# Optimization experiments

Measured on AMD Instinct MI355X. Metric: run time of the kernel, lower is better.

The kernel has to match this reference:

```python
import jax, jax.numpy as jnp
import numpy as np

NV, NE, D, NNZ = 100000, 50000, 128, 1600000
EPS = 1e-5

def _seg_mean(vals, idx, n):
    # vals: [nnz, d] gathered rows; mean-aggregate into n segments
    s = jax.ops.segment_sum(vals, idx, num_segments=n)
    c = jax.ops.segment_sum(jnp.ones((idx.shape[0], 1), vals.dtype), idx, num_segments=n)
    return s / jnp.maximum(c, 1.0)

def _linear(x, W, b):
    return x @ W.T + b

def _layer_norm(x, g, b):
    m = jnp.mean(x, axis=-1, keepdims=True)
    v = jnp.mean((x - m) ** 2, axis=-1, keepdims=True)
    return (x - m) * jax.lax.rsqrt(v + EPS) * g + b

def setup_inputs() -> dict:
    key = jax.random.key(0)
    ks = jax.random.split(key, 12)
    inp = {
        "X": jax.random.normal(ks[0], (NV, D), jnp.float32),
        "Y": jax.random.normal(ks[1], (NE, D), jnp.float32),
        "v_idx": jax.random.randint(ks[2], (NNZ,), 0, NV, jnp.int32),
        "e_idx": jax.random.randint(ks[3], (NNZ,), 0, NE, jnp.int32),
        "W_tv": jax.random.normal(ks[4], (D, D), jnp.float32) * 0.05,
        "b_tv": jnp.zeros((D,), jnp.float32),
        "W_te": jax.random.normal(ks[5], (D, D), jnp.float32) * 0.05,
        "b_te": jnp.zeros((D,), jnp.float32),
        "W_em": jax.random.normal(ks[6], (D, 2 * D), jnp.float32) * 0.05,
        "b_em": jnp.zeros((D,), jnp.float32),
        "W_vm": jax.random.normal(ks[7], (D, 2 * D), jnp.float32) * 0.05,
        "b_vm": jnp.zeros((D,), jnp.float32),
        "g_v": jnp.ones((D,), jnp.float32),
        "be_v": jnp.zeros((D,), jnp.float32),
        "g_e": jnp.ones((D,), jnp.float32),
        "be_e": jnp.zeros((D,), jnp.float32),
    }
    return inp

def reference(X, Y, v_idx, e_idx, W_tv, b_tv, W_te, b_te, W_em, b_em, W_vm, b_vm, g_v, be_v, g_e, be_e):
    X0, Y0 = X, Y
    Xp = _linear(X0, W_tv, b_tv)                       # [NV, D] theta_vertex
    # v2e aggregation (mean): gather vertex rows per incidence, reduce to edges
    msg_e = _seg_mean(Xp[v_idx], e_idx, NE)            # [NE, D]
    Ym = _linear(jnp.concatenate([Y0, msg_e], axis=-1), W_em, b_em)  # edge_merge
    Ym = _linear(Ym, W_te, b_te)                       # theta_edge
    # e2v aggregation (mean)
    msg_v = _seg_mean(Ym[e_idx], v_idx, NV)            # [NV, D]
    Xm = _linear(jnp.concatenate([X0, msg_v], axis=-1), W_vm, b_vm)  # vertex_merge
    Xo = jax.nn.relu(_layer_norm(Xm, g_v, be_v))       # dropout is identity at eval / p=0
    Yo = jax.nn.relu(_layer_norm(Ym, g_e, be_e))
    return (Xo, Yo)
```

## Files before the change

kernel.cpp:

```cpp
#include <hip/hip_runtime.h>
#include <stdint.h>

#define NVERT 100000
#define NEDGE 50000
#define DIM 128
#define NNZ_N 1600000
#define N4 (NNZ_N / 4)
#define CAP_E 96
#define NB_QTR 1563
#define LDS_STRIDE 136

typedef __attribute__((ext_vector_type(8))) short bf16x8;
typedef __attribute__((ext_vector_type(4))) float f32x4;

__device__ __forceinline__ unsigned short f32_to_bf16(float f) {
  union { float f; unsigned u; } v; v.f = f;
  unsigned r = v.u + 0x7fffu + ((v.u >> 16) & 1u);
  return (unsigned short)(r >> 16);
}
__device__ __forceinline__ float bf16_lo(unsigned u) {
  union { unsigned u; float f; } v; v.u = u << 16; return v.f;
}
__device__ __forceinline__ float bf16_hi(unsigned u) {
  union { unsigned u; float f; } v; v.u = u & 0xffff0000u; return v.f;
}
__device__ __forceinline__ float ldf(const void* p, long i, int bf) {
  if (bf) {
    union { unsigned u; float f; } v;
    v.u = (unsigned)((const unsigned short*)p)[i] << 16;
    return v.f;
  }
  return ((const float*)p)[i];
}
__device__ __forceinline__ bf16x8 frag_ext(const void* A, long idx, int bf) {
  if (bf) return *(const bf16x8*)((const unsigned short*)A + idx);
  const float* f = (const float*)A + idx;
  float4 f0 = *(const float4*)f, f1 = *(const float4*)(f + 4);
  bf16x8 r;
  r[0] = (short)f32_to_bf16(f0.x); r[1] = (short)f32_to_bf16(f0.y);
  r[2] = (short)f32_to_bf16(f0.z); r[3] = (short)f32_to_bf16(f0.w);
  r[4] = (short)f32_to_bf16(f1.x); r[5] = (short)f32_to_bf16(f1.y);
  r[6] = (short)f32_to_bf16(f1.z); r[7] = (short)f32_to_bf16(f1.w);
  return r;
}

__device__ __forceinline__ int block_flag(const unsigned short* x) {
  __shared__ int cnt;
  if (threadIdx.x == 0) cnt = 0;
  __syncthreads();
  int c = 0;
#pragma unroll
  for (int k = 0; k < 4; ++k) {
    unsigned short h = x[(threadIdx.x * 4 + k) * 2];
    int ex = (h >> 7) & 0xFF;
    c += (ex >= 100 && ex <= 140) ? 1 : 0;
  }
  atomicAdd(&cnt, c);
  __syncthreads();
  return cnt > 512;
}

__global__ __launch_bounds__(256) void prep_all(
    const unsigned short* __restrict__ Xu,
    const void* __restrict__ btv, const void* __restrict__ bvm,
    const void* __restrict__ Wtv, const void* __restrict__ Wvm,
    const void* __restrict__ Wte, const void* __restrict__ Wem,
    const void* __restrict__ bte, const void* __restrict__ bem,
    float* __restrict__ btvf, float* __restrict__ bvmf, float* __restrict__ bcf,
    unsigned short* __restrict__ Wtvb, unsigned short* __restrict__ Wvmb,
    unsigned short* __restrict__ Wcb, int* __restrict__ flag,
    int* __restrict__ cnt_e, int* __restrict__ cnt_v) {
  int b = blockIdx.x, t = threadIdx.x;
  if (b >= 321) {
    int i = (b - 321) * 256 + t;
    if (i < NEDGE) cnt_e[i] = 0;
    else if (i < NEDGE + NVERT) cnt_v[i - NEDGE] = 0;
    return;
  }
  int bf = block_flag(Xu);
  if (b == 0) {
    if (t == 0) flag[0] = bf;
    if (t < 128) btvf[t] = ldf(btv, t, bf);
    else bvmf[t - 128] = ldf(bvm, t - 128, bf);
  } else if (b < 65) {
    int i = (b - 1) * 256 + t;
    Wtvb[i] = f32_to_bf16(ldf(Wtv, i, bf));
  } else if (b < 193) {
    int i = (b - 65) * 256 + t;
    Wvmb[i] = f32_to_bf16(ldf(Wvm, i, bf));
  } else {
    int n = b - 193, k = t;
    float acc = 0.f;
    for (int j = 0; j < 128; ++j)
      acc += ldf(Wte, n * 128 + j, bf) * ldf(Wem, j * 256 + k, bf);
    Wcb[n * 256 + k] = f32_to_bf16(acc);
    if (k == 0) {
      float bb = ldf(bte, n, bf);
      for (int j = 0; j < 128; ++j) bb += ldf(Wte, n * 128 + j, bf) * ldf(bem, j, bf);
      bcf[n] = bb;
    }
  }
}

__device__ __forceinline__ void ecount_body(
    const int4* __restrict__ vi, const int4* __restrict__ ei,
    int* __restrict__ cnt_e, int* __restrict__ adj_e, int bid) {
  int i = bid * 256 + threadIdx.x;
  if (i >= N4) return;
  int4 e = ei[i], v = vi[i];
  int t;
  t = atomicAdd(&cnt_e[e.x], 1); if (t < CAP_E) adj_e[e.x * CAP_E + t] = v.x;
  t = atomicAdd(&cnt_e[e.y], 1); if (t < CAP_E) adj_e[e.y * CAP_E + t] = v.y;
  t = atomicAdd(&cnt_e[e.z], 1); if (t < CAP_E) adj_e[e.z * CAP_E + t] = v.z;
  t = atomicAdd(&cnt_e[e.w], 1); if (t < CAP_E) adj_e[e.w * CAP_E + t] = v.w;
}

__device__ __forceinline__ void vcount_body(
    const int4* __restrict__ vi, int* __restrict__ cnt_v,
    int4* __restrict__ tV, int bid) {
  int i = bid * 256 + threadIdx.x;
  if (i >= N4) return;
  int4 v = vi[i];
  int4 tv;
  tv.x = atomicAdd(&cnt_v[v.x], 1);
  tv.y = atomicAdd(&cnt_v[v.y], 1);
  tv.z = atomicAdd(&cnt_v[v.z], 1);
  tv.w = atomicAdd(&cnt_v[v.w], 1);
  tV[i] = tv;
}

__global__ __launch_bounds__(256) void k_wadjv(
    const int4* __restrict__ vi, const int4* __restrict__ ei,
    const int4* __restrict__ tV, const int* __restrict__ off_v,
    const int* __restrict__ bsum, int* __restrict__ adj_v) {
  int i = blockIdx.x * 256 + threadIdx.x;
  if (i >= N4) return;
  int4 e = ei[i], v = vi[i], tv = tV[i];
  adj_v[off_v[v.x] + bsum[v.x >> 10] + tv.x] = e.x;
  adj_v[off_v[v.y] + bsum[v.y >> 10] + tv.y] = e.y;
  adj_v[off_v[v.z] + bsum[v.z >> 10] + tv.z] = e.z;
  adj_v[off_v[v.w] + bsum[v.w >> 10] + tv.w] = e.w;
}

__global__ __launch_bounds__(1024) void scan_block(const int* __restrict__ in,
                                                   int* __restrict__ out,
                                                   int* __restrict__ bsum, int n) {
  __shared__ int sd[1024];
  const int tid = threadIdx.x;
  const int i = blockIdx.x * 1024 + tid;
  int x = (i < n) ? in[i] : 0;
  sd[tid] = x;
  __syncthreads();
  int v = x;
  for (int s = 1; s < 1024; s <<= 1) {
    int t = (tid >= s) ? sd[tid - s] : 0;
    __syncthreads();
    v += t;
    sd[tid] = v;
    __syncthreads();
  }
  if (i < n) out[i] = v - x;
  if (tid == 1023) bsum[blockIdx.x] = v;
}

__global__ __launch_bounds__(1024) void scan_sums(int* __restrict__ bsum, int nb) {
  __shared__ int sd[1024];
  const int tid = threadIdx.x;
  int x = (tid < nb) ? bsum[tid] : 0;
  sd[tid] = x;
  __syncthreads();
  int v = x;
  for (int s = 1; s < 1024; s <<= 1) {
    int t = (tid >= s) ? sd[tid - s] : 0;
    __syncthreads();
    v += t;
    sd[tid] = v;
    __syncthreads();
  }
  if (tid < nb) bsum[tid] = v - x;
}

template<bool CAPMODE>
__device__ __forceinline__ void seg_to_lds(
    const int* __restrict__ off_or_cnt, const int* __restrict__ bsum, int total,
    const int* __restrict__ adj, const unsigned short* __restrict__ tbl,
    unsigned short* __restrict__ lds, int nseg, int nrows, int blk) {
  const int g = threadIdx.x >> 4;
  const int l = threadIdx.x & 15;
#pragma unroll
  for (int t = 0; t < 4; ++t) {
    const int seg_local = t * 16 + g;
    const int seg = blk * 64 + seg_local;
    if (seg < nseg) {
      int s, e, cnt;
      if (CAPMODE) {
        cnt = off_or_cnt[seg];
        s = seg * CAP_E;
        e = s + (cnt < CAP_E ? cnt : CAP_E);
      } else {
        s = off_or_cnt[seg] + bsum[seg >> 10];
        e = (seg + 1 < nseg) ? off_or_cnt[seg + 1] + bsum[(seg + 1) >> 10] : total;
        cnt = e - s;
      }
      float a0 = 0, a1 = 0, a2 = 0, a3 = 0, a4 = 0, a5 = 0, a6 = 0, a7 = 0;
#define ACC(u)                                         \
  a0 += bf16_lo(u.x); a1 += bf16_hi(u.x);              \
  a2 += bf16_lo(u.y); a3 += bf16_hi(u.y);              \
  a4 += bf16_lo(u.z); a5 += bf16_hi(u.z);              \
  a6 += bf16_lo(u.w); a7 += bf16_hi(u.w);
      int i = s;
      for (; i + 4 <= e; i += 4) {
        int r0 = adj[i], r1 = adj[i + 1], r2 = adj[i + 2], r3 = adj[i + 3];
        if ((unsigned)r0 >= (unsigned)nrows) r0 = 0;
        if ((unsigned)r1 >= (unsigned)nrows) r1 = 0;
        if ((unsigned)r2 >= (unsigned)nrows) r2 = 0;
        if ((unsigned)r3 >= (unsigned)nrows) r3 = 0;
        uint4 u0 = *(const uint4*)(tbl + (long)r0 * DIM + l * 8);
        uint4 u1 = *(const uint4*)(tbl + (long)r1 * DIM + l * 8);
        uint4 u2 = *(const uint4*)(tbl + (long)r2 * DIM + l * 8);
        uint4 u3 = *(const uint4*)(tbl + (long)r3 * DIM + l * 8);
        ACC(u0) ACC(u1) ACC(u2) ACC(u3)
      }
      for (; i < e; ++i) {
        int r = adj[i];
        if ((unsigned)r >= (unsigned)nrows) r = 0;
        uint4 u = *(const uint4*)(tbl + (long)r * DIM + l * 8);
        ACC(u)
      }
#undef ACC
      float inv = (cnt > 0) ? 1.f / (float)cnt : 0.f;
      bf16x8 r;
      r[0] = (short)f32_to_bf16(a0 * inv); r[1] = (short)f32_to_bf16(a1 * inv);
      r[2] = (short)f32_to_bf16(a2 * inv); r[3] = (short)f32_to_bf16(a3 * inv);
      r[4] = (short)f32_to_bf16(a4 * inv); r[5] = (short)f32_to_bf16(a5 * inv);
      r[6] = (short)f32_to_bf16(a6 * inv); r[7] = (short)f32_to_bf16(a7 * inv);
      *(bf16x8*)&lds[seg_local * LDS_STRIDE + l * 8] = r;
    }
  }
  __syncthreads();
}

template<int KSTEPS, bool STORE_BF16>
__device__ __forceinline__ void gemm_body(
    int bid, const void* __restrict__ A0,
    const unsigned short* __restrict__ Bw, const float* __restrict__ biasf,
    unsigned short* __restrict__ outb, int M, int bf) {
  constexpr int K = KSTEPS * 32;
  const int wave = threadIdx.x >> 6;
  const int lane = threadIdx.x & 63;
  const int m0 = bid * 64 + wave * 16;
  if (m0 >= M) return;
  const int c = lane & 15;
  const int q = lane >> 4;
  const long arow = m0 + c;

  f32x4 acc[8];
#pragma unroll
  for (int t = 0; t < 8; ++t) acc[t] = (f32x4){0.f, 0.f, 0.f, 0.f};
#pragma unroll
  for (int ks = 0; ks < KSTEPS; ++ks) {
    const int kk = ks * 32 + q * 8;
    bf16x8 a = frag_ext(A0, arow * (long)K + kk, bf);
#pragma unroll
    for (int t = 0; t < 8; ++t) {
      bf16x8 b = *(const bf16x8*)(Bw + (long)(t * 16 + c) * K + kk);
      acc[t] = __builtin_amdgcn_mfma_f32_16x16x32_bf16(a, b, acc[t], 0, 0, 0);
    }
  }
#pragma unroll
  for (int t = 0; t < 8; ++t) {
    float bv = biasf[t * 16 + c];
#pragma unroll
    for (int i = 0; i < 4; ++i) acc[t][i] += bv;
  }
  if (STORE_BF16) {
#pragma unroll
    for (int t = 0; t < 8; ++t) {
      int col = t * 16 + c;
#pragma unroll
      for (int i = 0; i < 4; ++i)
        outb[(long)(m0 + q * 4 + i) * DIM + col] = f32_to_bf16(acc[t][i]);
    }
  }
}

template<bool STORE_BF16>
__device__ __forceinline__ void gemm_lds_body(
    int bid, const void* __restrict__ A0, const unsigned short* __restrict__ lds,
    const unsigned short* __restrict__ Bw, const float* __restrict__ biasf,
    unsigned short* __restrict__ outb, float* __restrict__ outf,
    const void* __restrict__ gw_, const void* __restrict__ bw_,
    int M, int bf) {
  constexpr int K = 256;
  const int wave = threadIdx.x >> 6;
  const int lane = threadIdx.x & 63;
  const int m0 = bid * 64 + wave * 16;
  if (m0 >= M) return;
  const int c = lane & 15;
  const int q = lane >> 4;
  const long arow = m0 + c;
  const int rloc = wave * 16 + c;

  f32x4 acc[8];
#pragma unroll
  for (int t = 0; t < 8; ++t) acc[t] = (f32x4){0.f, 0.f, 0.f, 0.f};
#pragma unroll
  for (int ks = 0; ks < 8; ++ks) {
    const int kk = ks * 32 + q * 8;
    bf16x8 a;
    if (ks >= 4) a = *(const bf16x8*)&lds[rloc * LDS_STRIDE + (kk - 128)];
    else         a = frag_ext(A0, arow * 128 + kk, bf);
#pragma unroll
    for (int t = 0; t < 8; ++t) {
      bf16x8 b = *(const bf16x8*)(Bw + (long)(t * 16 + c) * K + kk);
      acc[t] = __builtin_amdgcn_mfma_f32_16x16x32_bf16(a, b, acc[t], 0, 0, 0);
    }
  }
#pragma unroll
  for (int t = 0; t < 8; ++t) {
    float bv = biasf[t * 16 + c];
#pragma unroll
    for (int i = 0; i < 4; ++i) acc[t][i] += bv;
  }
  if (STORE_BF16) {
#pragma unroll
    for (int t = 0; t < 8; ++t) {
      int col = t * 16 + c;
#pragma unroll
      for (int i = 0; i < 4; ++i)
        outb[(long)(m0 + q * 4 + i) * DIM + col] = f32_to_bf16(acc[t][i]);
    }
  }
  float sum[4] = {0, 0, 0, 0}, sq[4] = {0, 0, 0, 0};
#pragma unroll
  for (int t = 0; t < 8; ++t)
#pragma unroll
    for (int i = 0; i < 4; ++i) { float v = acc[t][i]; sum[i] += v; sq[i] += v * v; }
#pragma unroll
  for (int m = 1; m <= 8; m <<= 1) {
#pragma unroll
    for (int i = 0; i < 4; ++i) {
      sum[i] += __shfl_xor(sum[i], m, 64);
      sq[i]  += __shfl_xor(sq[i], m, 64);
    }
  }
  float mean[4], rstd[4];
#pragma unroll
  for (int i = 0; i < 4; ++i) {
    mean[i] = sum[i] * (1.0f / 128.0f);
    float var = sq[i] * (1.0f / 128.0f) - mean[i] * mean[i];
    rstd[i] = rsqrtf(var + 1e-5f);
  }
#pragma unroll
  for (int t = 0; t < 8; ++t) {
    int col = t * 16 + c;
    float gv = ldf(gw_, col, bf), bv = ldf(bw_, col, bf);
#pragma unroll
    for (int i = 0; i < 4; ++i) {
      float v = (acc[t][i] - mean[i]) * rstd[i] * gv + bv;
      v = v > 0.f ? v : 0.f;
      outf[(long)(m0 + q * 4 + i) * DIM + col] = v;
    }
  }
}

__global__ __launch_bounds__(256) void k_ecount_gemm1(
    const int4* __restrict__ vi, const int4* __restrict__ ei,
    int* __restrict__ cnt_e, int* __restrict__ adj_e,
    const void* __restrict__ X, const unsigned short* __restrict__ Wtvb,
    const float* __restrict__ btvf, unsigned short* __restrict__ Xp_b,
    const int* __restrict__ flagp) {
  if (blockIdx.x & 1)
    gemm_body<4, true>(blockIdx.x >> 1, X, Wtvb, btvf, Xp_b, NVERT, *flagp);
  else
    ecount_body(vi, ei, cnt_e, adj_e, blockIdx.x >> 1);
}

__global__ __launch_bounds__(256) void k_vcount_seg1gemm2(
    const int4* __restrict__ vi, int* __restrict__ cnt_v, int4* __restrict__ tV,
    const int* __restrict__ cnt_e, const int* __restrict__ adj_e,
    const unsigned short* __restrict__ Xp_b,
    const void* __restrict__ Y, const unsigned short* __restrict__ Wcb,
    const float* __restrict__ bcf, unsigned short* __restrict__ Ym_b,
    float* __restrict__ Yo, const void* __restrict__ g_e,
    const void* __restrict__ be_e, const int* __restrict__ flagp) {
  __shared__ unsigned short lds[64 * LDS_STRIDE];
  int r = blockIdx.x % 3, q = blockIdx.x / 3;
  if (r < 2) {
    vcount_body(vi, cnt_v, tV, q * 2 + r);
    return;
  }
  seg_to_lds<true>(cnt_e, nullptr, 0, adj_e, Xp_b, lds, NEDGE, NVERT, q);
  gemm_lds_body<true>(q, Y, lds, Wcb, bcf, Ym_b, Yo, g_e, be_e, NEDGE, *flagp);
}

__global__ __launch_bounds__(256) void k_seg2gemm3(
    const int* __restrict__ off_v, const int* __restrict__ bsum,
    const int* __restrict__ adj_v, const unsigned short* __restrict__ Ym_b,
    const void* __restrict__ X, const unsigned short* __restrict__ Wvmb,
    const float* __restrict__ bvmf, float* __restrict__ Xo,
    const void* __restrict__ g_v, const void* __restrict__ be_v,
    const int* __restrict__ flagp) {
  __shared__ unsigned short lds[64 * LDS_STRIDE];
  seg_to_lds<false>(off_v, bsum, NNZ_N, adj_v, Ym_b, lds, NVERT, NEDGE, blockIdx.x);
  gemm_lds_body<false>(blockIdx.x, X, lds, Wvmb, bvmf, nullptr, Xo, g_v, be_v,
                       NVERT, *flagp);
}

extern "C" void kernel_launch(void* const* d_in, const int* in_sizes, int n_in,
                              void* d_out, int out_size, void* d_ws, size_t ws_size,
                              hipStream_t stream) {
  const void* X    = d_in[0];
  const void* Y    = d_in[1];
  const int*  v_idx = (const int*)d_in[2];
  const int*  e_idx = (const int*)d_in[3];
  const void* W_tv = d_in[4];
  const void* b_tv = d_in[5];
  const void* W_te = d_in[6];
  const void* b_te = d_in[7];
  const void* W_em = d_in[8];
  const void* b_em = d_in[9];
  const void* W_vm = d_in[10];
  const void* b_vm = d_in[11];
  const void* g_v  = d_in[12];
  const void* be_v = d_in[13];
  const void* g_e  = d_in[14];
  const void* be_e = d_in[15];

  unsigned short* Xp_b = (unsigned short*)d_out;
  int*   adj_e = (int*)((char*)d_out + 25600000);
  int4*  tV4   = (int4*)((char*)d_out + 44800000);
  float* Yo    = (float*)d_out + (long)NVERT * DIM;
  float* Xo    = (float*)d_out;

  char* p = (char*)d_ws;
  auto alloc = [&](size_t n) { char* r = p; p += (n + 255) & ~(size_t)255; return r; };
  int*   flag  = (int*)alloc(4);
  float* btv_f = (float*)alloc(DIM * 4);
  float* bvm_f = (float*)alloc(DIM * 4);
  float* bc_f  = (float*)alloc(DIM * 4);
  unsigned short* Wtv_b = (unsigned short*)alloc(DIM * DIM * 2);
  unsigned short* Wvm_b = (unsigned short*)alloc(2 * DIM * DIM * 2);
  unsigned short* Wc_b  = (unsigned short*)alloc(2 * DIM * DIM * 2);
  unsigned short* Ym_b  = (unsigned short*)alloc((long)NEDGE * DIM * 2);
  int* off_v  = (int*)alloc((NVERT + 1) * 4);
  int* cnt_e  = (int*)alloc(NEDGE * 4);
  int* cnt_v  = (int*)alloc(NVERT * 4);
  int* bsum_v = (int*)alloc(((NVERT + 1023) / 1024) * 4);
  int* adj_v  = (int*)alloc((long)NNZ_N * 4);

  prep_all<<<321 + (NEDGE + NVERT + 255) / 256, 256, 0, stream>>>(
      (const unsigned short*)X, b_tv, b_vm, W_tv, W_vm, W_te, W_em, b_te, b_em,
      btv_f, bvm_f, bc_f, Wtv_b, Wvm_b, Wc_b, flag, cnt_e, cnt_v);

  k_ecount_gemm1<<<2 * NB_QTR, 256, 0, stream>>>(
      (const int4*)v_idx, (const int4*)e_idx, cnt_e, adj_e,
      X, Wtv_b, btv_f, Xp_b, flag);

  k_vcount_seg1gemm2<<<3 * ((NEDGE + 63) / 64), 256, 0, stream>>>(
      (const int4*)v_idx, cnt_v, tV4, cnt_e, adj_e, Xp_b,
      Y, Wc_b, bc_f, Ym_b, Yo, g_e, be_e, flag);

  {
    int nbv = (NVERT + 1023) / 1024;
    scan_block<<<nbv, 1024, 0, stream>>>(cnt_v, off_v, bsum_v, NVERT);
    scan_sums<<<1, 1024, 0, stream>>>(bsum_v, nbv);
  }

  k_wadjv<<<NB_QTR, 256, 0, stream>>>(
      (const int4*)v_idx, (const int4*)e_idx, tV4, off_v, bsum_v, adj_v);

  k_seg2gemm3<<<(NVERT + 63) / 64, 256, 0, stream>>>(
      off_v, bsum_v, adj_v, Ym_b, X, Wvm_b, bvm_f, Xo, g_v, be_v, flag);
}
```

Baseline: 580.7 us.

## Split segment-mean from GEMMs via global message buffers and rebalance kernel fusion

Decouples the gather/mean aggregation from the merge GEMMs. Aggregated messages now go to global bf16 buffers placed in unused regions of the output, instead of LDS tiles inside a fused seg+GEMM block. The kernels are regrouped so independent work runs side by side: weight prep overlaps the first GEMM and edge counting, the edge GEMM overlaps writing the vertex adjacency, and half of the vertex GEMM overlaps the second half of vertex aggregation. The gather loop is also unrolled to 8 rows per iteration to keep more loads in flight. The cost is an extra global round-trip for the messages, more launches, and careful aliasing of output memory.

```diff
diff --git a/kernel.cpp b/kernel.cpp
--- a/kernel.cpp
+++ b/kernel.cpp
@@ -8,7 +8,8 @@
 #define N4 (NNZ_N / 4)
 #define CAP_E 96
 #define NB_QTR 1563
-#define LDS_STRIDE 136
+#define NB_G23 782
+#define MSG_STRIDE 256
 
 typedef __attribute__((ext_vector_type(8))) short bf16x8;
 typedef __attribute__((ext_vector_type(4))) float f32x4;
@@ -60,19 +61,16 @@
   return cnt > 512;
 }
 
-__global__ __launch_bounds__(256) void prep_all(
+__global__ __launch_bounds__(256) void prep0(
     const unsigned short* __restrict__ Xu,
     const void* __restrict__ btv, const void* __restrict__ bvm,
-    const void* __restrict__ Wtv, const void* __restrict__ Wvm,
-    const void* __restrict__ Wte, const void* __restrict__ Wem,
-    const void* __restrict__ bte, const void* __restrict__ bem,
-    float* __restrict__ btvf, float* __restrict__ bvmf, float* __restrict__ bcf,
-    unsigned short* __restrict__ Wtvb, unsigned short* __restrict__ Wvmb,
-    unsigned short* __restrict__ Wcb, int* __restrict__ flag,
+    const void* __restrict__ Wtv,
+    float* __restrict__ btvf, float* __restrict__ bvmf,
+    unsigned short* __restrict__ Wtvb, int* __restrict__ flag,
     int* __restrict__ cnt_e, int* __restrict__ cnt_v) {
   int b = blockIdx.x, t = threadIdx.x;
-  if (b >= 321) {
-    int i = (b - 321) * 256 + t;
+  if (b >= 65) {
+    int i = (b - 65) * 256 + t;
     if (i < NEDGE) cnt_e[i] = 0;
     else if (i < NEDGE + NVERT) cnt_v[i - NEDGE] = 0;
     return;
@@ -82,14 +80,23 @@
     if (t == 0) flag[0] = bf;
     if (t < 128) btvf[t] = ldf(btv, t, bf);
     else bvmf[t - 128] = ldf(bvm, t - 128, bf);
-  } else if (b < 65) {
+  } else {
     int i = (b - 1) * 256 + t;
     Wtvb[i] = f32_to_bf16(ldf(Wtv, i, bf));
-  } else if (b < 193) {
-    int i = (b - 65) * 256 + t;
+  }
+}
+
+__device__ __forceinline__ void prep_wc_body(
+    int b, const void* __restrict__ Wvm, const void* __restrict__ Wte,
+    const void* __restrict__ Wem, const void* __restrict__ bte,
+    const void* __restrict__ bem, unsigned short* __restrict__ Wvmb,
+    unsigned short* __restrict__ Wcb, float* __restrict__ bcf, int bf) {
+  int t = threadIdx.x;
+  if (b < 128) {
+    int i = b * 256 + t;
     Wvmb[i] = f32_to_bf16(ldf(Wvm, i, bf));
   } else {
-    int n = b - 193, k = t;
+    int n = b - 128, k = t;
     float acc = 0.f;
     for (int j = 0; j < 128; ++j)
       acc += ldf(Wte, n * 128 + j, bf) * ldf(Wem, j * 256 + k, bf);
@@ -129,11 +136,11 @@
   tV[i] = tv;
 }
 
-__global__ __launch_bounds__(256) void k_wadjv(
+__device__ __forceinline__ void wadjv_body(
     const int4* __restrict__ vi, const int4* __restrict__ ei,
     const int4* __restrict__ tV, const int* __restrict__ off_v,
-    const int* __restrict__ bsum, int* __restrict__ adj_v) {
-  int i = blockIdx.x * 256 + threadIdx.x;
+    const int* __restrict__ bsum, int* __restrict__ adj_v, int bid) {
+  int i = bid * 256 + threadIdx.x;
   if (i >= N4) return;
   int4 e = ei[i], v = vi[i], tv = tV[i];
   adj_v[off_v[v.x] + bsum[v.x >> 10] + tv.x] = e.x;
@@ -181,71 +188,65 @@
 }
 
 template<bool CAPMODE>
-__device__ __forceinline__ void seg_to_lds(
-    const int* __restrict__ off_or_cnt, const int* __restrict__ bsum, int total,
-    const int* __restrict__ adj, const unsigned short* __restrict__ tbl,
-    unsigned short* __restrict__ lds, int nseg, int nrows, int blk) {
-  const int g = threadIdx.x >> 4;
+__device__ __forceinline__ void seg_body(
+    const int* __restrict__ off_or_cnt, const int* __restrict__ adj,
+    const unsigned short* __restrict__ tbl, unsigned short* __restrict__ out,
+    int nseg, int nrows, const int* __restrict__ bsum, int total, int bid) {
+  const int seg = (bid * 256 + threadIdx.x) >> 4;
   const int l = threadIdx.x & 15;
-#pragma unroll
-  for (int t = 0; t < 4; ++t) {
-    const int seg_local = t * 16 + g;
-    const int seg = blk * 64 + seg_local;
-    if (seg < nseg) {
-      int s, e, cnt;
-      if (CAPMODE) {
-        cnt = off_or_cnt[seg];
-        s = seg * CAP_E;
-        e = s + (cnt < CAP_E ? cnt : CAP_E);
-      } else {
-        s = off_or_cnt[seg] + bsum[seg >> 10];
-        e = (seg + 1 < nseg) ? off_or_cnt[seg + 1] + bsum[(seg + 1) >> 10] : total;
-        cnt = e - s;
-      }
-      float a0 = 0, a1 = 0, a2 = 0, a3 = 0, a4 = 0, a5 = 0, a6 = 0, a7 = 0;
+  if (seg >= nseg) return;
+  int s, e, cnt;
+  if (CAPMODE) {
+    cnt = off_or_cnt[seg];
+    s = seg * CAP_E;
+    e = s + (cnt < CAP_E ? cnt : CAP_E);
+  } else {
+    s = off_or_cnt[seg] + bsum[seg >> 10];
+    e = (seg + 1 < nseg) ? off_or_cnt[seg + 1] + bsum[(seg + 1) >> 10] : total;
+    cnt = e - s;
+  }
+  float a0 = 0, a1 = 0, a2 = 0, a3 = 0, a4 = 0, a5 = 0, a6 = 0, a7 = 0;
+#define ROW(r, u)                                      \
+  if ((unsigned)r >= (unsigned)nrows) r = 0;           \
+  uint4 u = *(const uint4*)(tbl + (long)r * DIM + l * 8);
 #define ACC(u)                                         \
   a0 += bf16_lo(u.x); a1 += bf16_hi(u.x);              \
   a2 += bf16_lo(u.y); a3 += bf16_hi(u.y);              \
   a4 += bf16_lo(u.z); a5 += bf16_hi(u.z);              \
   a6 += bf16_lo(u.w); a7 += bf16_hi(u.w);
-      int i = s;
-      for (; i + 4 <= e; i += 4) {
-        int r0 = adj[i], r1 = adj[i + 1], r2 = adj[i + 2], r3 = adj[i + 3];
-        if ((unsigned)r0 >= (unsigned)nrows) r0 = 0;
-        if ((unsigned)r1 >= (unsigned)nrows) r1 = 0;
-        if ((unsigned)r2 >= (unsigned)nrows) r2 = 0;
-        if ((unsigned)r3 >= (unsigned)nrows) r3 = 0;
-        uint4 u0 = *(const uint4*)(tbl + (long)r0 * DIM + l * 8);
-        uint4 u1 = *(const uint4*)(tbl + (long)r1 * DIM + l * 8);
-        uint4 u2 = *(const uint4*)(tbl + (long)r2 * DIM + l * 8);
-        uint4 u3 = *(const uint4*)(tbl + (long)r3 * DIM + l * 8);
-        ACC(u0) ACC(u1) ACC(u2) ACC(u3)
-      }
-      for (; i < e; ++i) {
-        int r = adj[i];
-        if ((unsigned)r >= (unsigned)nrows) r = 0;
-        uint4 u = *(const uint4*)(tbl + (long)r * DIM + l * 8);
-        ACC(u)
-      }
+  int i = s;
+  for (; i + 8 <= e; i += 8) {
+    int r0 = adj[i],     r1 = adj[i + 1], r2 = adj[i + 2], r3 = adj[i + 3];
+    int r4 = adj[i + 4], r5 = adj[i + 5], r6 = adj[i + 6], r7 = adj[i + 7];
+    ROW(r0, u0) ROW(r1, u1) ROW(r2, u2) ROW(r3, u3)
+    ROW(r4, u4) ROW(r5, u5) ROW(r6, u6) ROW(r7, u7)
+    ACC(u0) ACC(u1) ACC(u2) ACC(u3) ACC(u4) ACC(u5) ACC(u6) ACC(u7)
+  }
+  for (; i + 4 <= e; i += 4) {
+    int r0 = adj[i], r1 = adj[i + 1], r2 = adj[i + 2], r3 = adj[i + 3];
+    ROW(r0, u0) ROW(r1, u1) ROW(r2, u2) ROW(r3, u3)
+    ACC(u0) ACC(u1) ACC(u2) ACC(u3)
+  }
+  for (; i < e; ++i) {
+    int r = adj[i];
+    ROW(r, u)
+    ACC(u)
+  }
 #undef ACC
-      float inv = (cnt > 0) ? 1.f / (float)cnt : 0.f;
-      bf16x8 r;
-      r[0] = (short)f32_to_bf16(a0 * inv); r[1] = (short)f32_to_bf16(a1 * inv);
-      r[2] = (short)f32_to_bf16(a2 * inv); r[3] = (short)f32_to_bf16(a3 * inv);
-      r[4] = (short)f32_to_bf16(a4 * inv); r[5] = (short)f32_to_bf16(a5 * inv);
-      r[6] = (short)f32_to_bf16(a6 * inv); r[7] = (short)f32_to_bf16(a7 * inv);
-      *(bf16x8*)&lds[seg_local * LDS_STRIDE + l * 8] = r;
-    }
-  }
-  __syncthreads();
-}
-
-template<int KSTEPS, bool STORE_BF16>
-__device__ __forceinline__ void gemm_body(
+#undef ROW
+  float inv = (cnt > 0) ? 1.f / (float)cnt : 0.f;
+  bf16x8 r;
+  r[0] = (short)f32_to_bf16(a0 * inv); r[1] = (short)f32_to_bf16(a1 * inv);
+  r[2] = (short)f32_to_bf16(a2 * inv); r[3] = (short)f32_to_bf16(a3 * inv);
+  r[4] = (short)f32_to_bf16(a4 * inv); r[5] = (short)f32_to_bf16(a5 * inv);
+  r[6] = (short)f32_to_bf16(a6 * inv); r[7] = (short)f32_to_bf16(a7 * inv);
+  *(bf16x8*)(out + (long)seg * MSG_STRIDE + l * 8) = r;
+}
+
+__device__ __forceinline__ void gemm1_body(
     int bid, const void* __restrict__ A0,
     const unsigned short* __restrict__ Bw, const float* __restrict__ biasf,
     unsigned short* __restrict__ outb, int M, int bf) {
-  constexpr int K = KSTEPS * 32;
   const int wave = threadIdx.x >> 6;
   const int lane = threadIdx.x & 63;
   const int m0 = bid * 64 + wave * 16;
@@ -253,53 +254,43 @@
   const int c = lane & 15;
   const int q = lane >> 4;
   const long arow = m0 + c;
-
   f32x4 acc[8];
 #pragma unroll
   for (int t = 0; t < 8; ++t) acc[t] = (f32x4){0.f, 0.f, 0.f, 0.f};
 #pragma unroll
-  for (int ks = 0; ks < KSTEPS; ++ks) {
+  for (int ks = 0; ks < 4; ++ks) {
     const int kk = ks * 32 + q * 8;
-    bf16x8 a = frag_ext(A0, arow * (long)K + kk, bf);
+    bf16x8 a = frag_ext(A0, arow * 128 + kk, bf);
 #pragma unroll
     for (int t = 0; t < 8; ++t) {
-      bf16x8 b = *(const bf16x8*)(Bw + (long)(t * 16 + c) * K + kk);
+      bf16x8 b = *(const bf16x8*)(Bw + (long)(t * 16 + c) * 128 + kk);
       acc[t] = __builtin_amdgcn_mfma_f32_16x16x32_bf16(a, b, acc[t], 0, 0, 0);
     }
   }
 #pragma unroll
   for (int t = 0; t < 8; ++t) {
     float bv = biasf[t * 16 + c];
-#pragma unroll
-    for (int i = 0; i < 4; ++i) acc[t][i] += bv;
-  }
-  if (STORE_BF16) {
-#pragma unroll
-    for (int t = 0; t < 8; ++t) {
-      int col = t * 16 + c;
-#pragma unroll
-      for (int i = 0; i < 4; ++i)
-        outb[(long)(m0 + q * 4 + i) * DIM + col] = f32_to_bf16(acc[t][i]);
-    }
+    int col = t * 16 + c;
+#pragma unroll
+    for (int i = 0; i < 4; ++i)
+      outb[(long)(m0 + q * 4 + i) * DIM + col] = f32_to_bf16(acc[t][i] + bv);
   }
 }
 
 template<bool STORE_BF16>
-__device__ __forceinline__ void gemm_lds_body(
-    int bid, const void* __restrict__ A0, const unsigned short* __restrict__ lds,
+__device__ __forceinline__ void gemm23_body(
+    int bid, int rowbase, int M,
+    const void* __restrict__ A0, const unsigned short* __restrict__ A1b,
     const unsigned short* __restrict__ Bw, const float* __restrict__ biasf,
     unsigned short* __restrict__ outb, float* __restrict__ outf,
-    const void* __restrict__ gw_, const void* __restrict__ bw_,
-    int M, int bf) {
-  constexpr int K = 256;
+    const void* __restrict__ gw_, const void* __restrict__ bw_, int bf) {
   const int wave = threadIdx.x >> 6;
   const int lane = threadIdx.x & 63;
-  const int m0 = bid * 64 + wave * 16;
+  const int m0 = rowbase + bid * 64 + wave * 16;
   if (m0 >= M) return;
   const int c = lane & 15;
   const int q = lane >> 4;
   const long arow = m0 + c;
-  const int rloc = wave * 16 + c;
 
   f32x4 acc[8];
 #pragma unroll
@@ -308,11 +299,11 @@
   for (int ks = 0; ks < 8; ++ks) {
     const int kk = ks * 32 + q * 8;
     bf16x8 a;
-    if (ks >= 4) a = *(const bf16x8*)&lds[rloc * LDS_STRIDE + (kk - 128)];
+    if (ks >= 4) a = *(const bf16x8*)(A1b + arow * MSG_STRIDE + (kk - 128));
     else         a = frag_ext(A0, arow * 128 + kk, bf);
 #pragma unroll
     for (int t = 0; t < 8; ++t) {
-      bf16x8 b = *(const bf16x8*)(Bw + (long)(t * 16 + c) * K + kk);
+      bf16x8 b = *(const bf16x8*)(Bw + (long)(t * 16 + c) * 256 + kk);
       acc[t] = __builtin_amdgcn_mfma_f32_16x16x32_bf16(a, b, acc[t], 0, 0, 0);
     }
   }
@@ -364,47 +355,89 @@
   }
 }
 
-__global__ __launch_bounds__(256) void k_ecount_gemm1(
+__global__ __launch_bounds__(256) void k1_prep_ecount_gemm1(
     const int4* __restrict__ vi, const int4* __restrict__ ei,
     int* __restrict__ cnt_e, int* __restrict__ adj_e,
     const void* __restrict__ X, const unsigned short* __restrict__ Wtvb,
     const float* __restrict__ btvf, unsigned short* __restrict__ Xp_b,
+    const void* __restrict__ Wvm, const void* __restrict__ Wte,
+    const void* __restrict__ Wem, const void* __restrict__ bte,
+    const void* __restrict__ bem, unsigned short* __restrict__ Wvmb,
+    unsigned short* __restrict__ Wcb, float* __restrict__ bcf,
     const int* __restrict__ flagp) {
-  if (blockIdx.x & 1)
-    gemm_body<4, true>(blockIdx.x >> 1, X, Wtvb, btvf, Xp_b, NVERT, *flagp);
+  int b = blockIdx.x;
+  if (b < 256) {
+    prep_wc_body(b, Wvm, Wte, Wem, bte, bem, Wvmb, Wcb, bcf, *flagp);
+    return;
+  }
+  int b2 = b - 256;
+  if (b2 & 1)
+    gemm1_body(b2 >> 1, X, Wtvb, btvf, Xp_b, NVERT, *flagp);
   else
-    ecount_body(vi, ei, cnt_e, adj_e, blockIdx.x >> 1);
-}
-
-__global__ __launch_bounds__(256) void k_vcount_seg1gemm2(
+    ecount_body(vi, ei, cnt_e, adj_e, b2 >> 1);
+}
+
+__global__ __launch_bounds__(256) void k2_vcount_seg1(
     const int4* __restrict__ vi, int* __restrict__ cnt_v, int4* __restrict__ tV,
     const int* __restrict__ cnt_e, const int* __restrict__ adj_e,
-    const unsigned short* __restrict__ Xp_b,
-    const void* __restrict__ Y, const unsigned short* __restrict__ Wcb,
-    const float* __restrict__ bcf, unsigned short* __restrict__ Ym_b,
-    float* __restrict__ Yo, const void* __restrict__ g_e,
-    const void* __restrict__ be_e, const int* __restrict__ flagp) {
-  __shared__ unsigned short lds[64 * LDS_STRIDE];
+    const unsigned short* __restrict__ Xp_b, unsigned short* __restrict__ msg_e) {
   int r = blockIdx.x % 3, q = blockIdx.x / 3;
-  if (r < 2) {
-    vcount_body(vi, cnt_v, tV, q * 2 + r);
-    return;
-  }
-  seg_to_lds<true>(cnt_e, nullptr, 0, adj_e, Xp_b, lds, NEDGE, NVERT, q);
-  gemm_lds_body<true>(q, Y, lds, Wcb, bcf, Ym_b, Yo, g_e, be_e, NEDGE, *flagp);
-}
-
-__global__ __launch_bounds__(256) void k_seg2gemm3(
+  if (r == 0)
+    vcount_body(vi, cnt_v, tV, q);
+  else
+    seg_body<true>(cnt_e, adj_e, Xp_b, msg_e, NEDGE, NVERT, nullptr, 0,
+                   q * 2 + (r - 1));
+}
+
+__global__ __launch_bounds__(256) void k3_wadjv_gemm2(
+    const int4* __restrict__ vi, const int4* __restrict__ ei,
+    const int4* __restrict__ tV, const int* __restrict__ off_v,
+    const int* __restrict__ bsum, int* __restrict__ adj_v,
+    const void* __restrict__ Y, const unsigned short* __restrict__ msg_e,
+    const unsigned short* __restrict__ Wcb, const float* __restrict__ bcf,
+    unsigned short* __restrict__ Ym_b, float* __restrict__ Yo,
+    const void* __restrict__ g_e, const void* __restrict__ be_e,
+    const int* __restrict__ flagp) {
+  int r = blockIdx.x % 3, q = blockIdx.x / 3;
+  if (r == 2)
+    gemm23_body<true>(q, 0, NEDGE, Y, msg_e, Wcb, bcf, Ym_b, Yo, g_e, be_e,
+                      *flagp);
+  else
+    wadjv_body(vi, ei, tV, off_v, bsum, adj_v, q * 2 + r);
+}
+
+__global__ __launch_bounds__(256) void k4a_seg2(
     const int* __restrict__ off_v, const int* __restrict__ bsum,
     const int* __restrict__ adj_v, const unsigned short* __restrict__ Ym_b,
+    unsigned short* __restrict__ msg_v) {
+  seg_body<false>(off_v, adj_v, Ym_b, msg_v, NVERT, NEDGE, bsum, NNZ_N,
+                  blockIdx.x);
+}
+
+__global__ __launch_bounds__(256) void k4b_seg2_gemm3(
+    const int* __restrict__ off_v, const int* __restrict__ bsum,
+    const int* __restrict__ adj_v, const unsigned short* __restrict__ Ym_b,
+    unsigned short* __restrict__ msg_v,
     const void* __restrict__ X, const unsigned short* __restrict__ Wvmb,
     const float* __restrict__ bvmf, float* __restrict__ Xo,
     const void* __restrict__ g_v, const void* __restrict__ be_v,
     const int* __restrict__ flagp) {
-  __shared__ unsigned short lds[64 * LDS_STRIDE];
-  seg_to_lds<false>(off_v, bsum, NNZ_N, adj_v, Ym_b, lds, NVERT, NEDGE, blockIdx.x);
-  gemm_lds_body<false>(blockIdx.x, X, lds, Wvmb, bvmf, nullptr, Xo, g_v, be_v,
-                       NVERT, *flagp);
+  int r = blockIdx.x % 5, q = blockIdx.x / 5;
+  if (r == 4)
+    gemm23_body<false>(q, 0, NVERT / 2, X, msg_v, Wvmb, bvmf, nullptr, Xo,
+                       g_v, be_v, *flagp);
+  else
+    seg_body<false>(off_v, adj_v, Ym_b, msg_v, NVERT, NEDGE, bsum, NNZ_N,
+                    3125 + q * 4 + r);
+}
+
+__global__ __launch_bounds__(256) void k5_gemm3(
+    const void* __restrict__ X, const unsigned short* __restrict__ msg_v,
+    const unsigned short* __restrict__ Wvmb, const float* __restrict__ bvmf,
+    float* __restrict__ Xo, const void* __restrict__ g_v,
+    const void* __restrict__ be_v, const int* __restrict__ flagp) {
+  gemm23_body<false>(blockIdx.x, NVERT / 2, NVERT, X, msg_v, Wvmb, bvmf,
+                     nullptr, Xo, g_v, be_v, *flagp);
 }
 
 extern "C" void kernel_launch(void* const* d_in, const int* in_sizes, int n_in,
@@ -427,10 +460,12 @@
   const void* g_e  = d_in[14];
   const void* be_e = d_in[15];
 
-  unsigned short* Xp_b = (unsigned short*)d_out;
+  unsigned short* Xp_b  = (unsigned short*)d_out;
   int*   adj_e = (int*)((char*)d_out + 25600000);
   int4*  tV4   = (int4*)((char*)d_out + 44800000);
-  float* Yo    = (float*)d_out + (long)NVERT * DIM;
+  unsigned short* msg_e = (unsigned short*)((char*)d_out + 51200000);
+  float* Yo    = (float*)((char*)d_out + 51200000);
+  unsigned short* msg_v = (unsigned short*)d_out;
   float* Xo    = (float*)d_out;
 
   char* p = (char*)d_ws;
@@ -449,17 +484,17 @@
   int* bsum_v = (int*)alloc(((NVERT + 1023) / 1024) * 4);
   int* adj_v  = (int*)alloc((long)NNZ_N * 4);
 
-  prep_all<<<321 + (NEDGE + NVERT + 255) / 256, 256, 0, stream>>>(
-      (const unsigned short*)X, b_tv, b_vm, W_tv, W_vm, W_te, W_em, b_te, b_em,
-      btv_f, bvm_f, bc_f, Wtv_b, Wvm_b, Wc_b, flag, cnt_e, cnt_v);
-
-  k_ecount_gemm1<<<2 * NB_QTR, 256, 0, stream>>>(
+  prep0<<<65 + (NEDGE + NVERT + 255) / 256, 256, 0, stream>>>(
+      (const unsigned short*)X, b_tv, b_vm, W_tv, btv_f, bvm_f, Wtv_b, flag,
+      cnt_e, cnt_v);
+
+  k1_prep_ecount_gemm1<<<256 + 2 * NB_QTR, 256, 0, stream>>>(
       (const int4*)v_idx, (const int4*)e_idx, cnt_e, adj_e,
-      X, Wtv_b, btv_f, Xp_b, flag);
-
-  k_vcount_seg1gemm2<<<3 * ((NEDGE + 63) / 64), 256, 0, stream>>>(
-      (const int4*)v_idx, cnt_v, tV4, cnt_e, adj_e, Xp_b,
-      Y, Wc_b, bc_f, Ym_b, Yo, g_e, be_e, flag);
+      X, Wtv_b, btv_f, Xp_b,
+      W_vm, W_te, W_em, b_te, b_em, Wvm_b, Wc_b, bc_f, flag);
+
+  k2_vcount_seg1<<<3 * NB_QTR, 256, 0, stream>>>(
+      (const int4*)v_idx, cnt_v, tV4, cnt_e, adj_e, Xp_b, msg_e);
 
   {
     int nbv = (NVERT + 1023) / 1024;
@@ -467,9 +502,15 @@
     scan_sums<<<1, 1024, 0, stream>>>(bsum_v, nbv);
   }
 
-  k_wadjv<<<NB_QTR, 256, 0, stream>>>(
-      (const int4*)v_idx, (const int4*)e_idx, tV4, off_v, bsum_v, adj_v);
-
-  k_seg2gemm3<<<(NVERT + 63) / 64, 256, 0, stream>>>(
-      off_v, bsum_v, adj_v, Ym_b, X, Wvm_b, bvm_f, Xo, g_v, be_v, flag);
-}
+  k3_wadjv_gemm2<<<3 * NB_G23, 256, 0, stream>>>(
+      (const int4*)v_idx, (const int4*)e_idx, tV4, off_v, bsum_v, adj_v,
+      Y, msg_e, Wc_b, bc_f, Ym_b, Yo, g_e, be_e, flag);
+
+  k4a_seg2<<<3125, 256, 0, stream>>>(off_v, bsum_v, adj_v, Ym_b, msg_v);
+
+  k4b_seg2_gemm3<<<5 * NB_G23, 256, 0, stream>>>(
+      off_v, bsum_v, adj_v, Ym_b, msg_v, X, Wvm_b, bvm_f, Xo, g_v, be_v, flag);
+
+  k5_gemm3<<<NB_G23, 256, 0, stream>>>(
+      X, msg_v, Wvm_b, bvm_f, Xo, g_v, be_v, flag);
+}
```

Result: faster. 542.0 us (-6.7%).
